# Kernel tuning notes

Measured on AMD Instinct MI355X. Metric: run time of the kernel, lower is better.

## Reference

```python
import math
import jax, jax.numpy as jnp
import numpy as np

B, S, D, H, E = 4, 1024, 1024, 16, 8
HD = D // H


def gelu_new(x):
    # BERT/GPT tanh-approx GELU (NewGELUActivation)
    c = math.sqrt(2.0 / math.pi)
    return 0.5 * x * (1.0 + jnp.tanh(c * (x + 0.044715 * x ** 3)))


def setup_inputs() -> dict:
    key = jax.random.key(0)
    ks = jax.random.split(key, 12)
    s = 0.02
    return {
        "x": jax.random.normal(ks[0], (B, S, D), jnp.float32),
        "Wq": jax.random.normal(ks[1], (D, D), jnp.float32) * s,
        "bq": jnp.zeros((D,), jnp.float32),
        "Wk": jax.random.normal(ks[2], (D, D), jnp.float32) * s,
        "bk": jnp.zeros((D,), jnp.float32),
        "Wv": jax.random.normal(ks[3], (D, D), jnp.float32) * s,
        "bv": jnp.zeros((D,), jnp.float32),
        "Wg": jax.random.normal(ks[4], (D, E), jnp.float32) * s,
        "bg": jnp.zeros((E,), jnp.float32),
        "W1": jax.random.normal(ks[5], (E, D, D), jnp.float32) * s,
        "b1": jnp.zeros((E, D), jnp.float32),
        "W2": jax.random.normal(ks[6], (E, D, D), jnp.float32) * s,
        "b2": jnp.zeros((E, D), jnp.float32),
    }


def reference(x, Wq, bq, Wk, bk, Wv, bv, Wg, bg, W1, b1, W2, b2):
    b = x.shape[0]
    # ---- Attention (faithful to original: no head transpose, so attention
    # is computed ACROSS HEADS per token: scores are [B,S,H,H]) ----
    Q = (x @ Wq + bq).reshape(b, -1, H, HD)
    K = (x @ Wk + bk).reshape(b, -1, H, HD)
    V = (x @ Wv + bv).reshape(b, -1, H, HD)
    scores = jnp.einsum('bsqd,bskd->bsqk', Q, K) / (HD ** 0.5)  # [B,S,H,H]
    attn = jax.nn.softmax(scores, axis=-1)
    out = jnp.einsum('bsqk,bskd->bsqd', attn, V)  # [B,S,H,HD]
    # torch: out.transpose(1,2).contiguous().view(B,-1,H*HD)
    a = jnp.transpose(out, (0, 2, 1, 3)).reshape(b, -1, D)  # [B,S,D]

    # ---- ComplexMoE: dense all-experts + sequence-mean gating ----
    gates = jax.nn.softmax(a.mean(axis=1) @ Wg + bg, axis=-1)  # [B,E]
    h = gelu_new(jnp.einsum('bsd,edh->bseh', a, W1) + b1)       # [B,S,E,D]
    eo = jnp.einsum('bseh,ehf->bsef', h, W2) + b2               # [B,S,E,D]
    return jnp.einsum('be,bsed->bsd', gates, eo)                # [B,S,D]
```

## Files before the change

kernel.cpp:

```cpp
#include <hip/hip_runtime.h>
#include <stdint.h>

#define AS1 __attribute__((address_space(1)))
#define AS3 __attribute__((address_space(3)))

typedef short v8s __attribute__((ext_vector_type(8)));
typedef float v4f __attribute__((ext_vector_type(4)));

__device__ __forceinline__ float b2f(unsigned short u) {
  return __uint_as_float(((unsigned int)u) << 16);
}
__device__ __forceinline__ unsigned short f2bu(float f) {
  unsigned int u = __float_as_uint(f);
  u += 0x7fffu + ((u >> 16) & 1u);
  return (unsigned short)(u >> 16);
}

__device__ __forceinline__ void gload16(const void* g, const void* l) {
  __builtin_amdgcn_global_load_lds(
      (const AS1 void*)(uintptr_t)g,
      (AS3 void*)(unsigned)(uintptr_t)l,
      16, 0, 0);
}

#define SB0 __builtin_amdgcn_sched_barrier(0)
#define BAR do { SB0; __builtin_amdgcn_s_barrier(); SB0; } while (0)
#define VMC4 asm volatile("s_waitcnt vmcnt(4)" ::: "memory")
#define VMC0 asm volatile("s_waitcnt vmcnt(0)" ::: "memory")

__global__ __launch_bounds__(256)
void transpose_cvt(const float* __restrict__ src, long long srcZ,
                   unsigned short* __restrict__ dst, long long dstZ, int ld_dst,
                   int K, int N)
{
  __shared__ float t[32][33];
  const int e = blockIdx.z;
  src += (long long)e * srcZ;
  dst += (long long)e * dstZ;
  const int k0 = blockIdx.y * 32, n0 = blockIdx.x * 32;
  const int tx = threadIdx.x & 31, ty = threadIdx.x >> 5;
#pragma unroll
  for (int r = 0; r < 32; r += 8)
    t[ty + r][tx] = src[(long long)(k0 + ty + r) * N + n0 + tx];
  __syncthreads();
#pragma unroll
  for (int r = 0; r < 32; r += 8) {
    const int n = ty + r;
    dst[(long long)(n0 + n) * ld_dst + k0 + tx] = f2bu(t[tx][n]);
  }
}

__global__ __launch_bounds__(256)
void cvt_f32_bf16(const float* __restrict__ src, unsigned short* __restrict__ dst, int n)
{
  const int i = (blockIdx.x * 256 + threadIdx.x) * 4;
  if (i >= n) return;
  float4 v = *(const float4*)(src + i);
  ushort4 o;
  o.x = f2bu(v.x); o.y = f2bu(v.y); o.z = f2bu(v.z); o.w = f2bu(v.w);
  *(ushort4*)(dst + i) = o;
}

template<int MH>
__device__ __forceinline__ void read_a(v8s af[4][2],
    const unsigned short* pa, int wm, int rswz)
{
#pragma unroll
  for (int i = 0; i < 4; ++i)
#pragma unroll
    for (int s = 0; s < 2; ++s)
      af[i][s] = *(const v8s*)(pa + MH*8192 + ((((wm*4 + i)*2 + s) << 9) | rswz));
}

template<int NH>
__device__ __forceinline__ void read_b(v8s bfr[2][2],
    const unsigned short* pb, int wn, int rswz)
{
#pragma unroll
  for (int j = 0; j < 2; ++j)
#pragma unroll
    for (int s = 0; s < 2; ++s)
      bfr[j][s] = *(const v8s*)(pb + NH*8192 + ((((wn*2 + j)*2 + s) << 9) | rswz));
}

template<int MH, int NH>
__device__ __forceinline__ void quad_mfma(v4f acc[8][4], v8s af[4][2], v8s bfr[2][2])
{
  __builtin_amdgcn_s_setprio(1);
#pragma unroll
  for (int i = 0; i < 4; ++i)
#pragma unroll
    for (int j = 0; j < 2; ++j)
#pragma unroll
      for (int s = 0; s < 2; ++s)
        acc[MH*4+i][NH*2+j] = __builtin_amdgcn_mfma_f32_16x16x32_bf16(
            af[i][s], bfr[j][s], acc[MH*4+i][NH*2+j], 0, 0, 0);
  __builtin_amdgcn_s_setprio(0);
}

#define STAGE(G, LD, LDSBASE, GROW0, KT) do { \
    gload16((G) + (long long)((GROW0) + sRow) * (LD) + (KT) + sCol, \
            (LDSBASE) + w*512); \
    gload16((G) + (long long)((GROW0) + 64 + sRow) * (LD) + (KT) + sCol, \
            (LDSBASE) + 4096 + w*512); \
  } while (0)

template<int EPI>
__global__ __launch_bounds__(512, 2)
void gemm256(const unsigned short* __restrict__ A, int lda,
             const unsigned short* __restrict__ Bt, int ldb,
             const float* __restrict__ bias,
             void* __restrict__ out0, unsigned short* __restrict__ pbs,
             int kLen, const float* __restrict__ gates)
{
  __shared__ __align__(16) unsigned short lds[65536];
  unsigned short* As0 = lds;
  unsigned short* As1 = lds + 16384;
  unsigned short* Bs0 = lds + 32768;
  unsigned short* Bs1 = lds + 49152;

  const int tid  = threadIdx.x;
  const int lane = tid & 63;
  const int w    = tid >> 6;
  const int wm   = w >> 2;
  const int wn   = w & 3;
  const int m0   = blockIdx.y * 256;
  const int n0   = blockIdx.x * 256;
  const int z    = blockIdx.z;
  const int kBase = (EPI == 3) ? z * kLen : 0;

  const int sRow = (w >> 1) * 16 + (lane >> 2);
  const int sCol = (w & 1) * 32 + (((lane & 3) * 8) ^ (((lane >> 5) & 1) << 4));
  const int rr   = lane & 15;
  const int kgrp = lane >> 4;
  const int rswz = (rr * 32 + kgrp * 8) ^ ((rr & 8) << 1);

  v4f acc[8][4] = {};
  v8s af[4][2], bfr[2][2];

  const int iters = kLen >> 7;

  STAGE(A,  lda, As0,        m0,       kBase);
  STAGE(A,  lda, As0 + 8192, m0 + 128, kBase);
  STAGE(Bt, ldb, Bs0,        n0,       kBase);
  STAGE(Bt, ldb, Bs0 + 8192, n0 + 128, kBase);
  STAGE(A,  lda, As1,        m0,       kBase + 64);
  STAGE(Bt, ldb, Bs1,        n0,       kBase + 64);
  VMC4;
  BAR;

  for (int it = 0; it < iters; ++it) {
    const bool nl = (it != iters - 1);
    const int kT1 = kBase + (2*it + 1) * 64;
    const int kT2 = kT1 + 64;
    const int kT3 = kT1 + 128;

    read_a<0>(af, As0, wm, rswz);
    read_b<1>(bfr, Bs0, wn, rswz);
    STAGE(A, lda, As1 + 8192, m0 + 128, kT1);
    BAR; quad_mfma<0,1>(acc, af, bfr); BAR;
    read_b<0>(bfr, Bs0, wn, rswz);
    STAGE(Bt, ldb, Bs1 + 8192, n0 + 128, kT1);
    BAR; quad_mfma<0,0>(acc, af, bfr); BAR;
    read_a<1>(af, As0, wm, rswz);
    if (nl) STAGE(A, lda, As0, m0, kT2);
    BAR; quad_mfma<1,0>(acc, af, bfr); BAR;
    read_b<1>(bfr, Bs0, wn, rswz);
    if (nl) STAGE(Bt, ldb, Bs0, n0, kT2);
    BAR; quad_mfma<1,1>(acc, af, bfr);
    if (nl) { VMC4; } else { VMC0; }
    BAR;
    read_a<0>(af, As1, wm, rswz);
    read_b<1>(bfr, Bs1, wn, rswz);
    if (nl) STAGE(A, lda, As0 + 8192, m0 + 128, kT2);
    BAR; quad_mfma<0,1>(acc, af, bfr); BAR;
    read_b<0>(bfr, Bs1, wn, rswz);
    if (nl) STAGE(Bt, ldb, Bs0 + 8192, n0 + 128, kT2);
    BAR; quad_mfma<0,0>(acc, af, bfr); BAR;
    read_a<1>(af, As1, wm, rswz);
    if (nl) STAGE(A, lda, As1, m0, kT3);
    BAR; quad_mfma<1,0>(acc, af, bfr); BAR;
    read_b<1>(bfr, Bs1, wn, rswz);
    if (nl) STAGE(Bt, ldb, Bs1, n0, kT3);
    BAR; quad_mfma<1,1>(acc, af, bfr);
    if (nl) { VMC4; } else { VMC0; }
    BAR;
  }

  const int lr4 = (lane >> 4) * 4;
  const int lc  = lane & 15;
  float gate = 0.f;
  if (EPI == 1) gate = gates[(m0 >> 10) * 8 + (n0 >> 10)];

#pragma unroll
  for (int mi = 0; mi < 8; ++mi) {
    const int rowb = m0 + (mi >> 2) * 128 + wm * 64 + (mi & 3) * 16 + lr4;
#pragma unroll
    for (int nj = 0; nj < 4; ++nj) {
      const int col = n0 + (nj >> 1) * 128 + wn * 32 + (nj & 1) * 16 + lc;
#pragma unroll
      for (int r = 0; r < 4; ++r) {
        const int row = rowb + r;
        float v = acc[mi][nj][r];
        if (EPI == 0) {
          v += bias[col];
          const int which = col >> 10;
          ((unsigned short*)out0)[(long long)which * 4194304 + (long long)row * 1024 + (col & 1023)] = f2bu(v);
        } else if (EPI == 1) {
          v += bias[col];
          float u = 0.7978845608028654f * (v + 0.044715f * v * v * v);
          u = fminf(fmaxf(u, -15.f), 15.f);
          float e2 = __expf(2.f * u);
          float th = (e2 - 1.f) / (e2 + 1.f);
          ((unsigned short*)out0)[(long long)row * 8192 + col] = f2bu(gate * 0.5f * v * (1.f + th));
        } else {
          if (z == 0) ((float*)out0)[(long long)row * 1024 + col] = v;
          else pbs[(long long)(z - 1) * 4194304 + (long long)row * 1024 + col] = f2bu(v);
        }
      }
    }
  }
}

__global__ __launch_bounds__(256)
void reduce3(float* __restrict__ out, const unsigned short* __restrict__ pb,
             const float* __restrict__ bias2)
{
  const int i = (blockIdx.x * 256 + threadIdx.x) * 4;
  const int b = i >> 20;
  const int n = i & 1023;
  float4 a = *(const float4*)(out + i);
  ushort4 p0 = *(const ushort4*)(pb + i);
  ushort4 p1 = *(const ushort4*)(pb + 4194304 + i);
  ushort4 p2 = *(const ushort4*)(pb + 8388608 + i);
  float4 bb = *(const float4*)(bias2 + b * 1024 + n);
  a.x += b2f(p0.x) + b2f(p1.x) + b2f(p2.x) + bb.x;
  a.y += b2f(p0.y) + b2f(p1.y) + b2f(p2.y) + bb.y;
  a.z += b2f(p0.z) + b2f(p1.z) + b2f(p2.z) + bb.z;
  a.w += b2f(p0.w) + b2f(p1.w) + b2f(p2.w) + bb.w;
  *(float4*)(out + i) = a;
}

__global__ __launch_bounds__(256)
void attn_kernel(const unsigned short* __restrict__ Qb,
                 const unsigned short* __restrict__ Kb,
                 const unsigned short* __restrict__ Vb,
                 unsigned short* __restrict__ a)
{
  const int token = blockIdx.x;
  const int b = token >> 10, s = token & 1023;
  __shared__ float Qs[16][65], Ks[16][65], Vs[16][65];
  __shared__ float attn_s[16][17];
  const int t = threadIdx.x;
  const long long base = (long long)token * 1024;

  {
    const int i0 = t * 4;
    const int hh = i0 >> 6, dd = i0 & 63;
    ushort4 qv = *(const ushort4*)(Qb + base + i0);
    ushort4 kv = *(const ushort4*)(Kb + base + i0);
    ushort4 vv = *(const ushort4*)(Vb + base + i0);
    Qs[hh][dd+0]=b2f(qv.x); Qs[hh][dd+1]=b2f(qv.y); Qs[hh][dd+2]=b2f(qv.z); Qs[hh][dd+3]=b2f(qv.w);
    Ks[hh][dd+0]=b2f(kv.x); Ks[hh][dd+1]=b2f(kv.y); Ks[hh][dd+2]=b2f(kv.z); Ks[hh][dd+3]=b2f(kv.w);
    Vs[hh][dd+0]=b2f(vv.x); Vs[hh][dd+1]=b2f(vv.y); Vs[hh][dd+2]=b2f(vv.z); Vs[hh][dd+3]=b2f(vv.w);
  }
  __syncthreads();

  const int q = t >> 4, k = t & 15;
  float sc = 0.f;
#pragma unroll
  for (int d = 0; d < 64; ++d) sc += Qs[q][d] * Ks[k][d];
  sc *= 0.125f;
  float mx = sc;
#pragma unroll
  for (int m = 1; m < 16; m <<= 1) mx = fmaxf(mx, __shfl_xor(mx, m, 64));
  float ex = __expf(sc - mx);
  float sum = ex;
#pragma unroll
  for (int m = 1; m < 16; m <<= 1) sum += __shfl_xor(sum, m, 64);
  attn_s[q][k] = ex / sum;
  __syncthreads();

  const int hd = t & 63;
  const int wv = t >> 6;
#pragma unroll
  for (int r = 0; r < 4; ++r) {
    const int qq = wv * 4 + r;
    float o = 0.f;
#pragma unroll
    for (int kk = 0; kk < 16; ++kk) o += attn_s[qq][kk] * Vs[kk][hd];
    a[(long long)b * 1048576 + (long long)(qq * 64 + (s >> 4)) * 1024 + (s & 15) * 64 + hd] = f2bu(o);
  }
}

__global__ __launch_bounds__(256)
void col_sum_part(const unsigned short* __restrict__ a, float* __restrict__ part)
{
  const int bx = blockIdx.x;
  const int b = bx >> 2;
  const int d = (bx & 3) * 256 + threadIdx.x;
  const int y = blockIdx.y;
  const unsigned short* p = a + (long long)b * 1048576 + (long long)y * 131072 + d;
  float s = 0.f;
  for (int i = 0; i < 128; ++i) s += b2f(p[i * 1024]);
  part[(y * 4 + b) * 1024 + d] = s;
}

__global__ __launch_bounds__(256)
void gates_bias2(const float* __restrict__ part,
                 const float* __restrict__ Wg,
                 const float* __restrict__ bg,
                 const float* __restrict__ b2,
                 float* __restrict__ gates,
                 float* __restrict__ bias2)
{
  __shared__ float am[4][1024];
  __shared__ float sg[4][8];
  const int t = threadIdx.x;

  for (int i = t; i < 4096; i += 256) {
    const int b = i >> 10, d = i & 1023;
    float s = 0.f;
#pragma unroll
    for (int y = 0; y < 8; ++y) s += part[(y * 4 + b) * 1024 + d];
    am[b][d] = s * (1.f / 1024.f);
  }
  __syncthreads();

  const int pair = t >> 3, subl = t & 7;
  const int b = pair >> 3, e = pair & 7;
  float s = 0.f;
  for (int d = subl * 128; d < subl * 128 + 128; ++d) s += am[b][d] * Wg[d * 8 + e];
#pragma unroll
  for (int m = 1; m < 8; m <<= 1) s += __shfl_xor(s, m, 64);
  if (subl == 0) sg[b][e] = s + bg[e];
  __syncthreads();

  if (t < 4) {
    float mx = -1e30f;
    for (int ee = 0; ee < 8; ++ee) mx = fmaxf(mx, sg[t][ee]);
    float g[8]; float ssum = 0.f;
    for (int ee = 0; ee < 8; ++ee) { g[ee] = __expf(sg[t][ee] - mx); ssum += g[ee]; }
    for (int ee = 0; ee < 8; ++ee) { sg[t][ee] = g[ee] / ssum; gates[t * 8 + ee] = sg[t][ee]; }
  }
  __syncthreads();

  for (int i = t; i < 4096; i += 256) {
    const int bb = i >> 10, n = i & 1023;
    float ss = 0.f;
#pragma unroll
    for (int ee = 0; ee < 8; ++ee) ss += sg[bb][ee] * b2[ee * 1024 + n];
    bias2[i] = ss;
  }
}

extern "C" void kernel_launch(void* const* d_in, const int* in_sizes, int n_in,
                              void* d_out, int out_size, void* d_ws, size_t ws_size,
                              hipStream_t stream) {
  const float* x  = (const float*)d_in[0];
  const float* Wq = (const float*)d_in[1];
  const float* bq = (const float*)d_in[2];
  const float* Wk = (const float*)d_in[3];
  const float* bk = (const float*)d_in[4];
  const float* Wv = (const float*)d_in[5];
  const float* bv = (const float*)d_in[6];
  const float* Wg = (const float*)d_in[7];
  const float* bg = (const float*)d_in[8];
  const float* W1 = (const float*)d_in[9];
  const float* b1 = (const float*)d_in[10];
  const float* W2 = (const float*)d_in[11];
  const float* b2 = (const float*)d_in[12];
  float* out = (float*)d_out;

  if (ws_size < (size_t)109300000) return;

  char* ws = (char*)d_ws;
  unsigned short* xb   = (unsigned short*)(ws + 0);
  unsigned short* Wqt  = (unsigned short*)(ws + 8388608);
  unsigned short* Qb   = (unsigned short*)(ws + 14680064);
  unsigned short* hs   = (unsigned short*)(ws + 0);
  unsigned short* abuf = (unsigned short*)(ws + 67108864);
  unsigned short* pbs  = (unsigned short*)(ws + 67108864);
  unsigned short* W1t  = (unsigned short*)(ws + 75497472);
  unsigned short* W2t  = (unsigned short*)(ws + 92274688);
  float* part  = (float*)(ws + 109051904);
  float* gates = (float*)(ws + 109051904 + 131072);
  float* bias2 = (float*)(ws + 109051904 + 131072 + 512);
  float* bqkv  = (float*)(ws + 109051904 + 131072 + 512 + 16384);

  dim3 tb(256);

  transpose_cvt<<<dim3(32,32,1), tb, 0, stream>>>(Wq, 0LL, Wqt,           0LL, 1024, 1024, 1024);
  transpose_cvt<<<dim3(32,32,1), tb, 0, stream>>>(Wk, 0LL, Wqt + 1048576, 0LL, 1024, 1024, 1024);
  transpose_cvt<<<dim3(32,32,1), tb, 0, stream>>>(Wv, 0LL, Wqt + 2097152, 0LL, 1024, 1024, 1024);
  transpose_cvt<<<dim3(32,32,8), tb, 0, stream>>>(W1, 1048576LL, W1t, 1048576LL, 1024, 1024, 1024);
  transpose_cvt<<<dim3(32,32,8), tb, 0, stream>>>(W2, 1048576LL, W2t, 1024LL,    8192, 1024, 1024);
  cvt_f32_bf16<<<4096, tb, 0, stream>>>(x, xb, 4194304);
  hipMemcpyAsync(bqkv,        bq, 4096, hipMemcpyDeviceToDevice, stream);
  hipMemcpyAsync(bqkv + 1024, bk, 4096, hipMemcpyDeviceToDevice, stream);
  hipMemcpyAsync(bqkv + 2048, bv, 4096, hipMemcpyDeviceToDevice, stream);

  gemm256<0><<<dim3(12,16,1), 512, 0, stream>>>(xb, 1024, Wqt, 1024, bqkv,
                                                Qb, nullptr, 1024, nullptr);
  attn_kernel<<<4096, tb, 0, stream>>>(Qb, Qb + 4194304, Qb + 8388608, abuf);
  col_sum_part<<<dim3(16,8), tb, 0, stream>>>(abuf, part);
  gates_bias2<<<1, tb, 0, stream>>>(part, Wg, bg, b2, gates, bias2);
  gemm256<1><<<dim3(32,16,1), 512, 0, stream>>>(abuf, 1024, W1t, 1024, b1,
                                                hs, nullptr, 1024, gates);
  gemm256<3><<<dim3(4,16,4), 512, 0, stream>>>(hs, 8192, W2t, 8192, nullptr,
                                               out, pbs, 2048, nullptr);
  reduce3<<<4096, tb, 0, stream>>>(out, pbs, bias2);
}
```

Baseline: 269.3 us.

## Double-buffer MFMA register fragments and reorder GEMM main-loop pipeline

```diff
diff --git a/kernel.cpp b/kernel.cpp
--- a/kernel.cpp
+++ b/kernel.cpp
@@ -23,9 +23,9 @@
       16, 0, 0);
 }
 
-#define SB0 __builtin_amdgcn_sched_barrier(0)
-#define BAR do { SB0; __builtin_amdgcn_s_barrier(); SB0; } while (0)
+#define BAR __builtin_amdgcn_s_barrier()
 #define VMC4 asm volatile("s_waitcnt vmcnt(4)" ::: "memory")
+#define VMC2 asm volatile("s_waitcnt vmcnt(2)" ::: "memory")
 #define VMC0 asm volatile("s_waitcnt vmcnt(0)" ::: "memory")
 
 __global__ __launch_bounds__(256)
@@ -97,13 +97,6 @@
             af[i][s], bfr[j][s], acc[MH*4+i][NH*2+j], 0, 0, 0);
   __builtin_amdgcn_s_setprio(0);
 }
-
-#define STAGE(G, LD, LDSBASE, GROW0, KT) do { \
-    gload16((G) + (long long)((GROW0) + sRow) * (LD) + (KT) + sCol, \
-            (LDSBASE) + w*512); \
-    gload16((G) + (long long)((GROW0) + 64 + sRow) * (LD) + (KT) + sCol, \
-            (LDSBASE) + 4096 + w*512); \
-  } while (0)
 
 template<int EPI>
 __global__ __launch_bounds__(512, 2)
@@ -134,57 +127,70 @@
   const int rr   = lane & 15;
   const int kgrp = lane >> 4;
   const int rswz = (rr * 32 + kgrp * 8) ^ ((rr & 8) << 1);
+  const int w512 = w * 512;
+
+  const unsigned short* pA0 = A + (long long)(m0       + sRow) * lda + kBase + sCol;
+  const unsigned short* pA1 = A + (long long)(m0 +  64 + sRow) * lda + kBase + sCol;
+  const unsigned short* pA2 = A + (long long)(m0 + 128 + sRow) * lda + kBase + sCol;
+  const unsigned short* pA3 = A + (long long)(m0 + 192 + sRow) * lda + kBase + sCol;
+  const unsigned short* pB0 = Bt + (long long)(n0       + sRow) * ldb + kBase + sCol;
+  const unsigned short* pB1 = Bt + (long long)(n0 +  64 + sRow) * ldb + kBase + sCol;
+  const unsigned short* pB2 = Bt + (long long)(n0 + 128 + sRow) * ldb + kBase + sCol;
+  const unsigned short* pB3 = Bt + (long long)(n0 + 192 + sRow) * ldb + kBase + sCol;
 
   v4f acc[8][4] = {};
-  v8s af[4][2], bfr[2][2];
+  v8s a0[4][2], a1[4][2], b0[2][2], b1[2][2];
 
   const int iters = kLen >> 7;
 
-  STAGE(A,  lda, As0,        m0,       kBase);
-  STAGE(A,  lda, As0 + 8192, m0 + 128, kBase);
-  STAGE(Bt, ldb, Bs0,        n0,       kBase);
-  STAGE(Bt, ldb, Bs0 + 8192, n0 + 128, kBase);
-  STAGE(A,  lda, As1,        m0,       kBase + 64);
-  STAGE(Bt, ldb, Bs1,        n0,       kBase + 64);
+  gload16(pA0,      As0 + w512);         gload16(pA1,      As0 + 4096 + w512);
+  gload16(pA2,      As0 + 8192 + w512);  gload16(pA3,      As0 + 12288 + w512);
+  gload16(pB0,      Bs0 + w512);         gload16(pB1,      Bs0 + 4096 + w512);
+  gload16(pB2,      Bs0 + 8192 + w512);  gload16(pB3,      Bs0 + 12288 + w512);
+  gload16(pA0 + 64, As1 + w512);         gload16(pA1 + 64, As1 + 4096 + w512);
+  gload16(pB0 + 64, Bs1 + w512);         gload16(pB1 + 64, Bs1 + 4096 + w512);
   VMC4;
   BAR;
+  read_a<0>(a0, As0, wm, rswz);
+  read_b<1>(b0, Bs0, wn, rswz);
 
   for (int it = 0; it < iters; ++it) {
     const bool nl = (it != iters - 1);
-    const int kT1 = kBase + (2*it + 1) * 64;
-    const int kT2 = kT1 + 64;
-    const int kT3 = kT1 + 128;
-
-    read_a<0>(af, As0, wm, rswz);
-    read_b<1>(bfr, Bs0, wn, rswz);
-    STAGE(A, lda, As1 + 8192, m0 + 128, kT1);
-    BAR; quad_mfma<0,1>(acc, af, bfr); BAR;
-    read_b<0>(bfr, Bs0, wn, rswz);
-    STAGE(Bt, ldb, Bs1 + 8192, n0 + 128, kT1);
-    BAR; quad_mfma<0,0>(acc, af, bfr); BAR;
-    read_a<1>(af, As0, wm, rswz);
-    if (nl) STAGE(A, lda, As0, m0, kT2);
-    BAR; quad_mfma<1,0>(acc, af, bfr); BAR;
-    read_b<1>(bfr, Bs0, wn, rswz);
-    if (nl) STAGE(Bt, ldb, Bs0, n0, kT2);
-    BAR; quad_mfma<1,1>(acc, af, bfr);
-    if (nl) { VMC4; } else { VMC0; }
+
+    read_b<0>(b1, Bs0, wn, rswz);
+    gload16(pA2 + 64, As1 + 8192 + w512); gload16(pA3 + 64, As1 + 12288 + w512);
+    BAR; quad_mfma<0,1>(acc, a0, b0); BAR;
+    read_a<1>(a1, As0, wm, rswz);
+    gload16(pB2 + 64, Bs1 + 8192 + w512); gload16(pB3 + 64, Bs1 + 12288 + w512);
+    BAR; quad_mfma<0,0>(acc, a0, b1); BAR;
+    if (nl) { gload16(pA0 + 128, As0 + w512); gload16(pA1 + 128, As0 + 4096 + w512); }
+    BAR; quad_mfma<1,0>(acc, a1, b1);
+    if (nl) { VMC2; } else { VMC0; }
     BAR;
-    read_a<0>(af, As1, wm, rswz);
-    read_b<1>(bfr, Bs1, wn, rswz);
-    if (nl) STAGE(A, lda, As0 + 8192, m0 + 128, kT2);
-    BAR; quad_mfma<0,1>(acc, af, bfr); BAR;
-    read_b<0>(bfr, Bs1, wn, rswz);
-    if (nl) STAGE(Bt, ldb, Bs0 + 8192, n0 + 128, kT2);
-    BAR; quad_mfma<0,0>(acc, af, bfr); BAR;
-    read_a<1>(af, As1, wm, rswz);
-    if (nl) STAGE(A, lda, As1, m0, kT3);
-    BAR; quad_mfma<1,0>(acc, af, bfr); BAR;
-    read_b<1>(bfr, Bs1, wn, rswz);
-    if (nl) STAGE(Bt, ldb, Bs1, n0, kT3);
-    BAR; quad_mfma<1,1>(acc, af, bfr);
-    if (nl) { VMC4; } else { VMC0; }
+    read_a<0>(a0, As1, wm, rswz);
+    read_b<1>(b1, Bs1, wn, rswz);
+    if (nl) { gload16(pB0 + 128, Bs0 + w512); gload16(pB1 + 128, Bs0 + 4096 + w512); }
+    BAR; quad_mfma<1,1>(acc, a1, b0); BAR;
+    read_b<0>(b0, Bs1, wn, rswz);
+    if (nl) { gload16(pA2 + 128, As0 + 8192 + w512); gload16(pA3 + 128, As0 + 12288 + w512); }
+    BAR; quad_mfma<0,1>(acc, a0, b1); BAR;
+    read_a<1>(a1, As1, wm, rswz);
+    if (nl) { gload16(pB2 + 128, Bs0 + 8192 + w512); gload16(pB3 + 128, Bs0 + 12288 + w512); }
+    BAR; quad_mfma<0,0>(acc, a0, b0); BAR;
+    if (nl) { gload16(pA0 + 192, As1 + w512); gload16(pA1 + 192, As1 + 4096 + w512); }
+    BAR; quad_mfma<1,0>(acc, a1, b0);
+    if (nl) { VMC2; }
     BAR;
+    if (nl) {
+      read_a<0>(a0, As0, wm, rswz);
+      read_b<1>(b0, Bs0, wn, rswz);
+      gload16(pB0 + 192, Bs1 + w512); gload16(pB1 + 192, Bs1 + 4096 + w512);
+    }
+    BAR; quad_mfma<1,1>(acc, a1, b1); BAR;
+    if (nl) {
+      pA0 += 128; pA1 += 128; pA2 += 128; pA3 += 128;
+      pB0 += 128; pB1 += 128; pB2 += 128; pB3 += 128;
+    }
   }
 
   const int lr4 = (lane >> 4) * 4;
```

Result: slower. 578.6 us (+114.9%).

## Restructure GEMM main loop into four phases with both B halves in registers

Applied to the files above, without the earlier changes.

```diff
diff --git a/kernel.cpp b/kernel.cpp
--- a/kernel.cpp
+++ b/kernel.cpp
@@ -23,8 +23,7 @@
       16, 0, 0);
 }
 
-#define SB0 __builtin_amdgcn_sched_barrier(0)
-#define BAR do { SB0; __builtin_amdgcn_s_barrier(); SB0; } while (0)
+#define BAR __builtin_amdgcn_s_barrier()
 #define VMC4 asm volatile("s_waitcnt vmcnt(4)" ::: "memory")
 #define VMC0 asm volatile("s_waitcnt vmcnt(0)" ::: "memory")
 
@@ -100,9 +99,9 @@
 
 #define STAGE(G, LD, LDSBASE, GROW0, KT) do { \
     gload16((G) + (long long)((GROW0) + sRow) * (LD) + (KT) + sCol, \
-            (LDSBASE) + w*512); \
+            (LDSBASE) + w512); \
     gload16((G) + (long long)((GROW0) + 64 + sRow) * (LD) + (KT) + sCol, \
-            (LDSBASE) + 4096 + w*512); \
+            (LDSBASE) + 4096 + w512); \
   } while (0)
 
 template<int EPI>
@@ -134,9 +133,10 @@
   const int rr   = lane & 15;
   const int kgrp = lane >> 4;
   const int rswz = (rr * 32 + kgrp * 8) ^ ((rr & 8) << 1);
+  const int w512 = w * 512;
 
   v4f acc[8][4] = {};
-  v8s af[4][2], bfr[2][2];
+  v8s af[4][2], blo[2][2], bhi[2][2];
 
   const int iters = kLen >> 7;
 
@@ -151,39 +151,39 @@
 
   for (int it = 0; it < iters; ++it) {
     const bool nl = (it != iters - 1);
-    const int kT1 = kBase + (2*it + 1) * 64;
-    const int kT2 = kT1 + 64;
-    const int kT3 = kT1 + 128;
+    const int k0t = kBase + it * 128;
+    const int kT1 = k0t + 64, kT2 = k0t + 128, kT3 = k0t + 192;
 
     read_a<0>(af, As0, wm, rswz);
-    read_b<1>(bfr, Bs0, wn, rswz);
-    STAGE(A, lda, As1 + 8192, m0 + 128, kT1);
-    BAR; quad_mfma<0,1>(acc, af, bfr); BAR;
-    read_b<0>(bfr, Bs0, wn, rswz);
+    read_b<0>(blo, Bs0, wn, rswz);
+    read_b<1>(bhi, Bs0, wn, rswz);
+    STAGE(A,  lda, As1 + 8192, m0 + 128, kT1);
     STAGE(Bt, ldb, Bs1 + 8192, n0 + 128, kT1);
-    BAR; quad_mfma<0,0>(acc, af, bfr); BAR;
+    BAR;
+    quad_mfma<0,0>(acc, af, blo);
+    quad_mfma<0,1>(acc, af, bhi);
+    BAR;
     read_a<1>(af, As0, wm, rswz);
-    if (nl) STAGE(A, lda, As0, m0, kT2);
-    BAR; quad_mfma<1,0>(acc, af, bfr); BAR;
-    read_b<1>(bfr, Bs0, wn, rswz);
-    if (nl) STAGE(Bt, ldb, Bs0, n0, kT2);
-    BAR; quad_mfma<1,1>(acc, af, bfr);
+    if (nl) { STAGE(A, lda, As0, m0, kT2); STAGE(Bt, ldb, Bs0, n0, kT2); }
+    BAR;
+    quad_mfma<1,0>(acc, af, blo);
+    quad_mfma<1,1>(acc, af, bhi);
     if (nl) { VMC4; } else { VMC0; }
     BAR;
     read_a<0>(af, As1, wm, rswz);
-    read_b<1>(bfr, Bs1, wn, rswz);
-    if (nl) STAGE(A, lda, As0 + 8192, m0 + 128, kT2);
-    BAR; quad_mfma<0,1>(acc, af, bfr); BAR;
-    read_b<0>(bfr, Bs1, wn, rswz);
-    if (nl) STAGE(Bt, ldb, Bs0 + 8192, n0 + 128, kT2);
-    BAR; quad_mfma<0,0>(acc, af, bfr); BAR;
+    read_b<0>(blo, Bs1, wn, rswz);
+    read_b<1>(bhi, Bs1, wn, rswz);
+    if (nl) { STAGE(A, lda, As0 + 8192, m0 + 128, kT2); STAGE(Bt, ldb, Bs0 + 8192, n0 + 128, kT2); }
+    BAR;
+    quad_mfma<0,0>(acc, af, blo);
+    quad_mfma<0,1>(acc, af, bhi);
+    BAR;
     read_a<1>(af, As1, wm, rswz);
-    if (nl) STAGE(A, lda, As1, m0, kT3);
-    BAR; quad_mfma<1,0>(acc, af, bfr); BAR;
-    read_b<1>(bfr, Bs1, wn, rswz);
-    if (nl) STAGE(Bt, ldb, Bs1, n0, kT3);
-    BAR; quad_mfma<1,1>(acc, af, bfr);
-    if (nl) { VMC4; } else { VMC0; }
+    if (nl) { STAGE(A, lda, As1, m0, kT3); STAGE(Bt, ldb, Bs1, n0, kT3); }
+    BAR;
+    quad_mfma<1,0>(acc, af, blo);
+    quad_mfma<1,1>(acc, af, bhi);
+    if (nl) VMC4;
     BAR;
   }
 
```

After: 269.5 us. About the same (+0.1%).
